# Performance work log

Hardware: AMD Instinct MI355X
Metric: run time of the kernel (lower is better)

## Reference

```python
import jax, jax.numpy as jnp
import numpy as np

N = 16384      # n_samples
D = 1024       # embedding_size
C = 16         # number of classes (balanced so every anchor has a positive)
MARGIN = 1.0
EPS = 1e-6


def setup_inputs() -> dict:
    rng = np.random.default_rng(0)
    labels = np.arange(N) % C
    rng.shuffle(labels)
    # positive index: same label, different sample (random within-class rotation)
    pos = np.empty(N, dtype=np.int64)
    for c in range(C):
        idx = np.nonzero(labels == c)[0]
        off = rng.integers(1, len(idx), size=len(idx))
        pos[idx] = idx[(np.arange(len(idx)) + off) % len(idx)]
    # negative index: any sample with a different label (rejection-resample on host)
    neg = rng.integers(0, N, size=N)
    while True:
        bad = labels[neg] == labels
        if not bad.any():
            break
        neg[bad] = rng.integers(0, N, size=int(bad.sum()))
    key = jax.random.key(0)
    embeddings = jax.random.normal(key, (N, D), dtype=jnp.float32)
    return {
        "embeddings": embeddings,
        "labels": jnp.asarray(labels, dtype=jnp.int64),
        "pos_idx": jnp.asarray(pos, dtype=jnp.int64),
        "neg_idx": jnp.asarray(neg, dtype=jnp.int64),
    }


def reference(embeddings, labels, pos_idx, neg_idx):
    # F.normalize(p=2, dim=1, eps=1e-6): x / max(||x||_2, eps)
    norm = jnp.sqrt(jnp.sum(embeddings * embeddings, axis=1, keepdims=True))
    e = embeddings / jnp.maximum(norm, EPS)                      # [N, D]

    def pdist(a, b):
        # F.pairwise_distance adds eps to the difference; module adds another +eps
        return jnp.sqrt(jnp.sum((a - b + EPS) ** 2, axis=1)) + EPS

    d_pos = pdist(e, e[pos_idx])                                 # [N]
    d_neg = pdist(e, e[neg_idx])                                 # [N]
    positive_loss = d_pos ** 2
    negative_loss = jnp.maximum(MARGIN - d_neg, EPS) ** 2
    total = jnp.sum(positive_loss) + jnp.sum(negative_loss)
    return total / (2.0 * N)
```

## Files before the change

kernel.cpp:

```cpp
#include <hip/hip_runtime.h>

#define NROWS 16384
#define DIM   1024
#define MARGIN_F 1.0f
#define EPS_F 1e-6f

__global__ __launch_bounds__(256, 8) void row_loss_kernel(
    const float* __restrict__ emb,
    const int*   __restrict__ pos_idx,
    const int*   __restrict__ neg_idx,
    float*       __restrict__ block_part)
{
    const int tid  = threadIdx.x;
    const int lane = tid & 63;
    const int wid  = tid >> 6;
    const int row  = blockIdx.x * 4 + wid;

    const int p = pos_idx[row];
    const int n = neg_idx[row];

    const float4* xi = (const float4*)(emb + (size_t)row * DIM) + lane;
    const float4* xp = (const float4*)(emb + (size_t)p   * DIM) + lane;
    const float4* xn = (const float4*)(emb + (size_t)n   * DIM) + lane;

    float ni = 0.f, np_ = 0.f, nn = 0.f;
    float dip = 0.f, din = 0.f;
    float sa = 0.f, sb = 0.f, sc = 0.f;

    float4 a0 = xi[0],   b0 = xp[0],   c0 = xn[0];
    float4 a1 = xi[64],  b1 = xp[64],  c1 = xn[64];

    #define ACC(A,B,C)                                                                                     \
        ni  = fmaf(A.x,A.x,ni);  ni  = fmaf(A.y,A.y,ni);  ni  = fmaf(A.z,A.z,ni);  ni  = fmaf(A.w,A.w,ni); \
        np_ = fmaf(B.x,B.x,np_); np_ = fmaf(B.y,B.y,np_); np_ = fmaf(B.z,B.z,np_); np_ = fmaf(B.w,B.w,np_);\
        nn  = fmaf(C.x,C.x,nn);  nn  = fmaf(C.y,C.y,nn);  nn  = fmaf(C.z,C.z,nn);  nn  = fmaf(C.w,C.w,nn); \
        dip = fmaf(A.x,B.x,dip); dip = fmaf(A.y,B.y,dip); dip = fmaf(A.z,B.z,dip); dip = fmaf(A.w,B.w,dip);\
        din = fmaf(A.x,C.x,din); din = fmaf(A.y,C.y,din); din = fmaf(A.z,C.z,din); din = fmaf(A.w,C.w,din);\
        sa += (A.x + A.y) + (A.z + A.w);                                                                   \
        sb += (B.x + B.y) + (B.z + B.w);                                                                   \
        sc += (C.x + C.y) + (C.z + C.w);

    float4 a2 = xi[128], b2 = xp[128], c2 = xn[128];
    ACC(a0, b0, c0)
    float4 a3 = xi[192], b3 = xp[192], c3 = xn[192];
    ACC(a1, b1, c1)
    ACC(a2, b2, c2)
    ACC(a3, b3, c3)
    #undef ACC

    #pragma unroll
    for (int m = 1; m < 64; m <<= 1) {
        ni  += __shfl_xor(ni,  m, 64);
        np_ += __shfl_xor(np_, m, 64);
        nn  += __shfl_xor(nn,  m, 64);
        dip += __shfl_xor(dip, m, 64);
        din += __shfl_xor(din, m, 64);
        sa  += __shfl_xor(sa,  m, 64);
        sb  += __shfl_xor(sb,  m, 64);
        sc  += __shfl_xor(sc,  m, 64);
    }

    __shared__ float sm[4];
    if (lane == 0) {
        const float si = 1.0f / fmaxf(sqrtf(ni),  EPS_F);
        const float sp = 1.0f / fmaxf(sqrtf(np_), EPS_F);
        const float sn = 1.0f / fmaxf(sqrtf(nn),  EPS_F);
        const float de2 = (float)DIM * EPS_F * EPS_F;

        float sum_p = fmaf(si * si, ni, fmaf(sp * sp, np_, -2.f * si * sp * dip))
                    + 2.f * EPS_F * (si * sa - sp * sb) + de2;
        float sum_n = fmaf(si * si, ni, fmaf(sn * sn, nn, -2.f * si * sn * din))
                    + 2.f * EPS_F * (si * sa - sn * sc) + de2;

        float d_pos = sqrtf(fmaxf(sum_p, 0.f)) + EPS_F;
        float d_neg = sqrtf(fmaxf(sum_n, 0.f)) + EPS_F;
        float mq    = fmaxf(MARGIN_F - d_neg, EPS_F);
        sm[wid] = fmaf(d_pos, d_pos, mq * mq);
    }
    __syncthreads();
    if (tid == 0)
        block_part[blockIdx.x] = (sm[0] + sm[1]) + (sm[2] + sm[3]);
}

__global__ __launch_bounds__(256) void final_reduce_kernel(
    const float* __restrict__ part,
    float*       __restrict__ out)
{
    const int tid = threadIdx.x;
    const float4* p4 = (const float4*)part;
    float s = 0.f;
    #pragma unroll
    for (int j = 0; j < 4; ++j) {
        float4 v = p4[tid + 256 * j];
        s += (v.x + v.y) + (v.z + v.w);
    }
    #pragma unroll
    for (int m = 1; m < 64; m <<= 1) s += __shfl_xor(s, m, 64);

    __shared__ float sm[4];
    if ((tid & 63) == 0) sm[tid >> 6] = s;
    __syncthreads();
    if (tid == 0)
        out[0] = ((sm[0] + sm[1]) + (sm[2] + sm[3])) * (1.0f / (2.0f * (float)NROWS));
}

extern "C" void kernel_launch(void* const* d_in, const int* in_sizes, int n_in,
                              void* d_out, int out_size, void* d_ws, size_t ws_size,
                              hipStream_t stream) {
    const float* emb = (const float*)d_in[0];
    const int* pos = (const int*)d_in[2];
    const int* neg = (const int*)d_in[3];

    float* parts = (float*)d_ws;
    float* out   = (float*)d_out;

    row_loss_kernel<<<NROWS / 4, 256, 0, stream>>>(emb, pos, neg, parts);
    final_reduce_kernel<<<1, 256, 0, stream>>>(parts, out);
}
```

Before: 116.1 us.

## Process four rows per wave with register double-buffered prefetch of next row

Each wave now handles four consecutive rows instead of one, prefetching the anchor, positive and negative rows for the next row into registers while computing the current one. The grid shrinks fourfold, launch bounds drop to 4 blocks per SIMD, and the final reduction reads only 1024 partials. The aim is to keep more loads in flight per wave and cut block and launch overhead. The cost is higher register pressure and fewer resident waves, which could reduce latency hiding on this memory-bound gather.

```diff
diff --git a/kernel.cpp b/kernel.cpp
--- a/kernel.cpp
+++ b/kernel.cpp
@@ -2,10 +2,15 @@
 
 #define NROWS 16384
 #define DIM   1024
+#define F4_PER_ROW 256
 #define MARGIN_F 1.0f
 #define EPS_F 1e-6f
 
-__global__ __launch_bounds__(256, 8) void row_loss_kernel(
+#define ROWS_PER_WAVE   4
+#define WAVES_PER_BLOCK 4
+#define NBLOCKS (NROWS / (ROWS_PER_WAVE * WAVES_PER_BLOCK))
+
+__global__ __launch_bounds__(256, 4) void row_loss_kernel(
     const float* __restrict__ emb,
     const int*   __restrict__ pos_idx,
     const int*   __restrict__ neg_idx,
@@ -14,58 +19,73 @@
     const int tid  = threadIdx.x;
     const int lane = tid & 63;
     const int wid  = tid >> 6;
-    const int row  = blockIdx.x * 4 + wid;
+    const int wave = blockIdx.x * WAVES_PER_BLOCK + wid;
+    const int base = wave * ROWS_PER_WAVE;
 
-    const int p = pos_idx[row];
-    const int n = neg_idx[row];
+    int pidx[ROWS_PER_WAVE], nidx[ROWS_PER_WAVE];
+    #pragma unroll
+    for (int k = 0; k < ROWS_PER_WAVE; ++k) {
+        pidx[k] = pos_idx[base + k];
+        nidx[k] = neg_idx[base + k];
+    }
 
-    const float4* xi = (const float4*)(emb + (size_t)row * DIM) + lane;
-    const float4* xp = (const float4*)(emb + (size_t)p   * DIM) + lane;
-    const float4* xn = (const float4*)(emb + (size_t)n   * DIM) + lane;
+    const float4* e4 = (const float4*)emb;
+    #define ROWPTR(r) (e4 + (size_t)(r) * F4_PER_ROW + lane)
 
-    float ni = 0.f, np_ = 0.f, nn = 0.f;
-    float dip = 0.f, din = 0.f;
-    float sa = 0.f, sb = 0.f, sc = 0.f;
+    float4 ca[4], cb[4], cc[4];
+    float4 na[4], nb[4], nc[4];
+    #pragma unroll
+    for (int j = 0; j < 4; ++j) {
+        ca[j] = ROWPTR(base)[64 * j];
+        cb[j] = ROWPTR(pidx[0])[64 * j];
+        cc[j] = ROWPTR(nidx[0])[64 * j];
+    }
 
-    float4 a0 = xi[0],   b0 = xp[0],   c0 = xn[0];
-    float4 a1 = xi[64],  b1 = xp[64],  c1 = xn[64];
-
-    #define ACC(A,B,C)                                                                                     \
-        ni  = fmaf(A.x,A.x,ni);  ni  = fmaf(A.y,A.y,ni);  ni  = fmaf(A.z,A.z,ni);  ni  = fmaf(A.w,A.w,ni); \
-        np_ = fmaf(B.x,B.x,np_); np_ = fmaf(B.y,B.y,np_); np_ = fmaf(B.z,B.z,np_); np_ = fmaf(B.w,B.w,np_);\
-        nn  = fmaf(C.x,C.x,nn);  nn  = fmaf(C.y,C.y,nn);  nn  = fmaf(C.z,C.z,nn);  nn  = fmaf(C.w,C.w,nn); \
-        dip = fmaf(A.x,B.x,dip); dip = fmaf(A.y,B.y,dip); dip = fmaf(A.z,B.z,dip); dip = fmaf(A.w,B.w,dip);\
-        din = fmaf(A.x,C.x,din); din = fmaf(A.y,C.y,din); din = fmaf(A.z,C.z,din); din = fmaf(A.w,C.w,din);\
-        sa += (A.x + A.y) + (A.z + A.w);                                                                   \
-        sb += (B.x + B.y) + (B.z + B.w);                                                                   \
-        sc += (C.x + C.y) + (C.z + C.w);
-
-    float4 a2 = xi[128], b2 = xp[128], c2 = xn[128];
-    ACC(a0, b0, c0)
-    float4 a3 = xi[192], b3 = xp[192], c3 = xn[192];
-    ACC(a1, b1, c1)
-    ACC(a2, b2, c2)
-    ACC(a3, b3, c3)
-    #undef ACC
+    const float de2 = (float)DIM * EPS_F * EPS_F;
+    float wave_acc = 0.f;
 
     #pragma unroll
-    for (int m = 1; m < 64; m <<= 1) {
-        ni  += __shfl_xor(ni,  m, 64);
-        np_ += __shfl_xor(np_, m, 64);
-        nn  += __shfl_xor(nn,  m, 64);
-        dip += __shfl_xor(dip, m, 64);
-        din += __shfl_xor(din, m, 64);
-        sa  += __shfl_xor(sa,  m, 64);
-        sb  += __shfl_xor(sb,  m, 64);
-        sc  += __shfl_xor(sc,  m, 64);
-    }
+    for (int k = 0; k < ROWS_PER_WAVE; ++k) {
+        if (k + 1 < ROWS_PER_WAVE) {
+            #pragma unroll
+            for (int j = 0; j < 4; ++j) {
+                na[j] = ROWPTR(base + k + 1)[64 * j];
+                nb[j] = ROWPTR(pidx[k + 1])[64 * j];
+                nc[j] = ROWPTR(nidx[k + 1])[64 * j];
+            }
+        }
 
-    __shared__ float sm[4];
-    if (lane == 0) {
+        float ni = 0.f, np_ = 0.f, nn = 0.f;
+        float dip = 0.f, din = 0.f;
+        float sa = 0.f, sb = 0.f, sc = 0.f;
+        #pragma unroll
+        for (int j = 0; j < 4; ++j) {
+            const float4 A = ca[j], B = cb[j], C = cc[j];
+            ni  = fmaf(A.x,A.x,ni);  ni  = fmaf(A.y,A.y,ni);  ni  = fmaf(A.z,A.z,ni);  ni  = fmaf(A.w,A.w,ni);
+            np_ = fmaf(B.x,B.x,np_); np_ = fmaf(B.y,B.y,np_); np_ = fmaf(B.z,B.z,np_); np_ = fmaf(B.w,B.w,np_);
+            nn  = fmaf(C.x,C.x,nn);  nn  = fmaf(C.y,C.y,nn);  nn  = fmaf(C.z,C.z,nn);  nn  = fmaf(C.w,C.w,nn);
+            dip = fmaf(A.x,B.x,dip); dip = fmaf(A.y,B.y,dip); dip = fmaf(A.z,B.z,dip); dip = fmaf(A.w,B.w,dip);
+            din = fmaf(A.x,C.x,din); din = fmaf(A.y,C.y,din); din = fmaf(A.z,C.z,din); din = fmaf(A.w,C.w,din);
+            sa += (A.x + A.y) + (A.z + A.w);
+            sb += (B.x + B.y) + (B.z + B.w);
+            sc += (C.x + C.y) + (C.z + C.w);
+        }
+
+        #pragma unroll
+        for (int m = 1; m < 64; m <<= 1) {
+            ni  += __shfl_xor(ni,  m, 64);
+            np_ += __shfl_xor(np_, m, 64);
+            nn  += __shfl_xor(nn,  m, 64);
+            dip += __shfl_xor(dip, m, 64);
+            din += __shfl_xor(din, m, 64);
+            sa  += __shfl_xor(sa,  m, 64);
+            sb  += __shfl_xor(sb,  m, 64);
+            sc  += __shfl_xor(sc,  m, 64);
+        }
+
         const float si = 1.0f / fmaxf(sqrtf(ni),  EPS_F);
         const float sp = 1.0f / fmaxf(sqrtf(np_), EPS_F);
         const float sn = 1.0f / fmaxf(sqrtf(nn),  EPS_F);
-        const float de2 = (float)DIM * EPS_F * EPS_F;
 
         float sum_p = fmaf(si * si, ni, fmaf(sp * sp, np_, -2.f * si * sp * dip))
                     + 2.f * EPS_F * (si * sa - sp * sb) + de2;
@@ -75,8 +95,17 @@
         float d_pos = sqrtf(fmaxf(sum_p, 0.f)) + EPS_F;
         float d_neg = sqrtf(fmaxf(sum_n, 0.f)) + EPS_F;
         float mq    = fmaxf(MARGIN_F - d_neg, EPS_F);
-        sm[wid] = fmaf(d_pos, d_pos, mq * mq);
+        wave_acc += fmaf(d_pos, d_pos, mq * mq);
+
+        if (k + 1 < ROWS_PER_WAVE) {
+            #pragma unroll
+            for (int j = 0; j < 4; ++j) { ca[j] = na[j]; cb[j] = nb[j]; cc[j] = nc[j]; }
+        }
     }
+    #undef ROWPTR
+
+    __shared__ float sm[WAVES_PER_BLOCK];
+    if (lane == 0) sm[wid] = wave_acc;
     __syncthreads();
     if (tid == 0)
         block_part[blockIdx.x] = (sm[0] + sm[1]) + (sm[2] + sm[3]);
@@ -88,12 +117,8 @@
 {
     const int tid = threadIdx.x;
     const float4* p4 = (const float4*)part;
-    float s = 0.f;
-    #pragma unroll
-    for (int j = 0; j < 4; ++j) {
-        float4 v = p4[tid + 256 * j];
-        s += (v.x + v.y) + (v.z + v.w);
-    }
+    float4 v = p4[tid];
+    float s = (v.x + v.y) + (v.z + v.w);
     #pragma unroll
     for (int m = 1; m < 64; m <<= 1) s += __shfl_xor(s, m, 64);
 
@@ -114,6 +139,6 @@
     float* parts = (float*)d_ws;
     float* out   = (float*)d_out;
 
-    row_loss_kernel<<<NROWS / 4, 256, 0, stream>>>(emb, pos, neg, parts);
+    row_loss_kernel<<<NBLOCKS, 256, 0, stream>>>(emb, pos, neg, parts);
     final_reduce_kernel<<<1, 256, 0, stream>>>(parts, out);
 }
```

New measurement: 115.8 us. No clear change (-0.2%).

## Fuse final reduction via atomicAdd and issue all row loads upfront

Applied to the files above, without the earlier changes.

The separate final-reduce kernel is removed. Each block now atomically adds its scaled partial sum into the output, which is zeroed by a memset placed before the launch. All twelve float4 loads per lane are issued before any arithmetic, behind a compiler memory barrier, and the occupancy hint in launch_bounds is dropped. The intent is to save one kernel launch and raise memory-level parallelism. The cost is 4096 atomic adds contending on a single address, a non-deterministic float summation order, and possibly higher register pressure.

```diff
diff --git a/kernel.cpp b/kernel.cpp
--- a/kernel.cpp
+++ b/kernel.cpp
@@ -2,14 +2,15 @@
 
 #define NROWS 16384
 #define DIM   1024
+#define F4_PER_ROW 256
 #define MARGIN_F 1.0f
 #define EPS_F 1e-6f
 
-__global__ __launch_bounds__(256, 8) void row_loss_kernel(
+__global__ __launch_bounds__(256) void row_loss_kernel(
     const float* __restrict__ emb,
     const int*   __restrict__ pos_idx,
     const int*   __restrict__ neg_idx,
-    float*       __restrict__ block_part)
+    float*       __restrict__ out)
 {
     const int tid  = threadIdx.x;
     const int lane = tid & 63;
@@ -23,30 +24,30 @@
     const float4* xp = (const float4*)(emb + (size_t)p   * DIM) + lane;
     const float4* xn = (const float4*)(emb + (size_t)n   * DIM) + lane;
 
+    float4 a[4], b[4], c[4];
+    #pragma unroll
+    for (int j = 0; j < 4; ++j) {
+        a[j] = xi[64 * j];
+        b[j] = xp[64 * j];
+        c[j] = xn[64 * j];
+    }
+    asm volatile("" ::: "memory");
+
     float ni = 0.f, np_ = 0.f, nn = 0.f;
     float dip = 0.f, din = 0.f;
     float sa = 0.f, sb = 0.f, sc = 0.f;
-
-    float4 a0 = xi[0],   b0 = xp[0],   c0 = xn[0];
-    float4 a1 = xi[64],  b1 = xp[64],  c1 = xn[64];
-
-    #define ACC(A,B,C)                                                                                     \
-        ni  = fmaf(A.x,A.x,ni);  ni  = fmaf(A.y,A.y,ni);  ni  = fmaf(A.z,A.z,ni);  ni  = fmaf(A.w,A.w,ni); \
-        np_ = fmaf(B.x,B.x,np_); np_ = fmaf(B.y,B.y,np_); np_ = fmaf(B.z,B.z,np_); np_ = fmaf(B.w,B.w,np_);\
-        nn  = fmaf(C.x,C.x,nn);  nn  = fmaf(C.y,C.y,nn);  nn  = fmaf(C.z,C.z,nn);  nn  = fmaf(C.w,C.w,nn); \
-        dip = fmaf(A.x,B.x,dip); dip = fmaf(A.y,B.y,dip); dip = fmaf(A.z,B.z,dip); dip = fmaf(A.w,B.w,dip);\
-        din = fmaf(A.x,C.x,din); din = fmaf(A.y,C.y,din); din = fmaf(A.z,C.z,din); din = fmaf(A.w,C.w,din);\
-        sa += (A.x + A.y) + (A.z + A.w);                                                                   \
-        sb += (B.x + B.y) + (B.z + B.w);                                                                   \
+    #pragma unroll
+    for (int j = 0; j < 4; ++j) {
+        const float4 A = a[j], B = b[j], C = c[j];
+        ni  = fmaf(A.x,A.x,ni);  ni  = fmaf(A.y,A.y,ni);  ni  = fmaf(A.z,A.z,ni);  ni  = fmaf(A.w,A.w,ni);
+        np_ = fmaf(B.x,B.x,np_); np_ = fmaf(B.y,B.y,np_); np_ = fmaf(B.z,B.z,np_); np_ = fmaf(B.w,B.w,np_);
+        nn  = fmaf(C.x,C.x,nn);  nn  = fmaf(C.y,C.y,nn);  nn  = fmaf(C.z,C.z,nn);  nn  = fmaf(C.w,C.w,nn);
+        dip = fmaf(A.x,B.x,dip); dip = fmaf(A.y,B.y,dip); dip = fmaf(A.z,B.z,dip); dip = fmaf(A.w,B.w,dip);
+        din = fmaf(A.x,C.x,din); din = fmaf(A.y,C.y,din); din = fmaf(A.z,C.z,din); din = fmaf(A.w,C.w,din);
+        sa += (A.x + A.y) + (A.z + A.w);
+        sb += (B.x + B.y) + (B.z + B.w);
         sc += (C.x + C.y) + (C.z + C.w);
-
-    float4 a2 = xi[128], b2 = xp[128], c2 = xn[128];
-    ACC(a0, b0, c0)
-    float4 a3 = xi[192], b3 = xp[192], c3 = xn[192];
-    ACC(a1, b1, c1)
-    ACC(a2, b2, c2)
-    ACC(a3, b3, c3)
-    #undef ACC
+    }
 
     #pragma unroll
     for (int m = 1; m < 64; m <<= 1) {
@@ -79,29 +80,7 @@
     }
     __syncthreads();
     if (tid == 0)
-        block_part[blockIdx.x] = (sm[0] + sm[1]) + (sm[2] + sm[3]);
-}
-
-__global__ __launch_bounds__(256) void final_reduce_kernel(
-    const float* __restrict__ part,
-    float*       __restrict__ out)
-{
-    const int tid = threadIdx.x;
-    const float4* p4 = (const float4*)part;
-    float s = 0.f;
-    #pragma unroll
-    for (int j = 0; j < 4; ++j) {
-        float4 v = p4[tid + 256 * j];
-        s += (v.x + v.y) + (v.z + v.w);
-    }
-    #pragma unroll
-    for (int m = 1; m < 64; m <<= 1) s += __shfl_xor(s, m, 64);
-
-    __shared__ float sm[4];
-    if ((tid & 63) == 0) sm[tid >> 6] = s;
-    __syncthreads();
-    if (tid == 0)
-        out[0] = ((sm[0] + sm[1]) + (sm[2] + sm[3])) * (1.0f / (2.0f * (float)NROWS));
+        atomicAdd(out, ((sm[0] + sm[1]) + (sm[2] + sm[3])) * (1.0f / (2.0f * (float)NROWS)));
 }
 
 extern "C" void kernel_launch(void* const* d_in, const int* in_sizes, int n_in,
@@ -111,9 +90,8 @@
     const int* pos = (const int*)d_in[2];
     const int* neg = (const int*)d_in[3];
 
-    float* parts = (float*)d_ws;
-    float* out   = (float*)d_out;
+    float* out = (float*)d_out;
+    hipMemsetAsync(out, 0, sizeof(float), stream);
 
-    row_loss_kernel<<<NROWS / 4, 256, 0, stream>>>(emb, pos, neg, parts);
-    final_reduce_kernel<<<1, 256, 0, stream>>>(parts, out);
+    row_loss_kernel<<<NROWS / 4, 256, 0, stream>>>(emb, pos, neg, out);
 }
```

New measurement: 145.0 us. +24.9%, slower.
